# Kernel optimization log

Measured on AMD Instinct MI355X. Metric: run time of the kernel, lower is better.

## Reference

```python
import jax, jax.numpy as jnp
import numpy as np

N = 50000      # graph nodes
E = 800000     # edges
R = 8          # relations
D = 128        # entity_dim == relation_dim == n_hidden
L = 2          # gnn layers
NE = 150000    # entity vocab
NEG_SLOPE = 0.01


def setup_inputs() -> dict:
    key = jax.random.key(0)
    ks = jax.random.split(key, 9)
    return {
        "node_ids": jax.random.randint(ks[0], (N,), 0, NE),
        "relation_ids": jax.random.randint(ks[1], (E,), 0, R),
        "src": jax.random.randint(ks[2], (E,), 0, N),
        "dst": jax.random.randint(ks[3], (E,), 0, N),
        "entity_table": jax.random.normal(ks[4], (NE, D), dtype=jnp.float32) * 0.1,
        "relation_table": jax.random.normal(ks[5], (R, D), dtype=jnp.float32) * 0.1,
        "relation_W": jax.random.normal(ks[6], (R, D, D), dtype=jnp.float32) * 0.1,
        "res_fc_W": jax.random.normal(ks[7], (L, D, D), dtype=jnp.float32) * 0.1,
        "res_fc2_W": jax.random.normal(ks[8], (L, D, D), dtype=jnp.float32) * 0.1,
    }


def _kgat_layer(h, efeat, rel, src, dst, relation_W, W1, W2):
    # project every node by every relation weight: (N, R, D)
    proj = jnp.einsum('nd,rde->nre', h, relation_W)
    t_r = proj[src, rel]            # (E, D)  W_r h_src
    h_r = proj[dst, rel]            # (E, D)  W_r h_dst
    # att = (W_r h_t)^T tanh(W_r h_dst + e_r)
    att = jnp.sum(t_r * jnp.tanh(h_r + efeat), axis=1)  # (E,)
    # edge softmax over incoming edges of each dst node
    m = jax.ops.segment_max(att, dst, num_segments=N)
    ex = jnp.exp(att - m[dst])
    s = jax.ops.segment_sum(ex, dst, num_segments=N)
    a = ex / s[dst]                 # (E,)
    # message = a * h_src, scatter-sum to dst
    h_nb = jax.ops.segment_sum(h[src] * a[:, None], dst, num_segments=N)  # (N, D)
    out = (jax.nn.leaky_relu((h + h_nb) @ W1.T, NEG_SLOPE)
           + jax.nn.leaky_relu((h * h_nb) @ W2.T, NEG_SLOPE))
    return h_nb, out


def reference(node_ids, relation_ids, src, dst, entity_table, relation_table,
              relation_W, res_fc_W, res_fc2_W):
    h = entity_table[node_ids]           # (N, D)
    efeat = relation_table[relation_ids]  # (E, D)
    cache = [h]
    for i in range(L):
        h, out = _kgat_layer(h, efeat, relation_ids, src, dst,
                             relation_W, res_fc_W[i], res_fc2_W[i])
        cache.append(out)
    return jnp.concatenate(cache, axis=1)  # (N, D*(L+1))
```

## Files before the change

kernel.cpp:

```cpp
#include <hip/hip_runtime.h>
#include <math.h>

#define DDIM 128
#define RREL 8

typedef _Float16 f16;
typedef __attribute__((ext_vector_type(2))) _Float16 h2;
typedef __attribute__((ext_vector_type(8))) _Float16 f16x8;
typedef __attribute__((ext_vector_type(4))) float f32x4;

static __device__ __forceinline__ unsigned short f2h(float f) {
    union { _Float16 h; unsigned short s; } c; c.h = (_Float16)f; return c.s;
}
static __device__ __forceinline__ h2 u2h(unsigned u) {
    union { unsigned u; h2 h; } c; c.u = u; return c.h;
}
static __device__ __forceinline__ unsigned h2u(h2 h) {
    union { unsigned u; h2 h; } c; c.h = h; return c.u;
}
static __device__ __forceinline__ float lrelu(float x) {
    return x > 0.0f ? x : 0.01f * x;
}
static __device__ __forceinline__ float tanh_fast(float x) {
    float e = __expf(2.0f * x);
    return 1.0f - 2.0f * __builtin_amdgcn_rcpf(e + 1.0f);
}

__global__ __launch_bounds__(256) void prep_weights(const float* __restrict__ relW,
                                                    const float* __restrict__ fcW,
                                                    const float* __restrict__ fc2W,
                                                    unsigned short* __restrict__ Wt,
                                                    unsigned short* __restrict__ Wq,
                                                    unsigned short* __restrict__ Wb1,
                                                    unsigned short* __restrict__ Wb2) {
    int i = blockIdx.x * 256 + threadIdx.x;
    const int NT = RREL * DDIM * DDIM;
    const int NF = 2 * DDIM * DDIM;
    if (i < NT) {
        float w = relW[i];
        int r = i >> 14;
        int d = (i >> 7) & 127;
        int e = i & 127;
        unsigned short h = f2h(w);
        Wt[(r << 14) + (e << 7) + d] = h;
        Wq[i] = h;
    } else if (i < NT + NF) {
        int j = i - NT;
        Wb1[j] = f2h(fcW[j]);
    } else if (i < NT + 2 * NF) {
        int j = i - NT - NF;
        Wb2[j] = f2h(fc2W[j]);
    }
}

__global__ __launch_bounds__(256) void gather_h0(const int* __restrict__ node_ids,
                                                 const float* __restrict__ etab,
                                                 unsigned short* __restrict__ hb0,
                                                 float* __restrict__ out, int N) {
    int i = blockIdx.x * 256 + threadIdx.x;
    if (i >= N * 32) return;
    int n = i >> 5;
    int c4 = (i & 31) * 4;
    float4 v = *(const float4*)(etab + (size_t)node_ids[n] * DDIM + c4);
    *(float4*)(out + (size_t)n * 384 + c4) = v;
    unsigned lo = (unsigned)f2h(v.x) | ((unsigned)f2h(v.y) << 16);
    unsigned hi = (unsigned)f2h(v.z) | ((unsigned)f2h(v.w) << 16);
    *(uint2*)(hb0 + (size_t)n * DDIM + c4) = make_uint2(lo, hi);
}

__global__ __launch_bounds__(256) void hist_k(const int* __restrict__ dst,
                                              int* __restrict__ counts, int E) {
    int i = blockIdx.x * 256 + threadIdx.x;
    if (i < E) atomicAdd(counts + dst[i], 1);
}

__global__ __launch_bounds__(256) void scan_a(const int* __restrict__ counts,
                                              int* __restrict__ tmp,
                                              int* __restrict__ part, int N) {
    __shared__ int sh[256];
    int i = blockIdx.x * 256 + threadIdx.x;
    int v = (i < N) ? counts[i] : 0;
    sh[threadIdx.x] = v;
    __syncthreads();
    #pragma unroll
    for (int o = 1; o < 256; o <<= 1) {
        int t = (threadIdx.x >= o) ? sh[threadIdx.x - o] : 0;
        __syncthreads();
        sh[threadIdx.x] += t;
        __syncthreads();
    }
    if (i < N) tmp[i] = sh[threadIdx.x];
    if (threadIdx.x == 255) part[blockIdx.x] = sh[255];
}

__global__ __launch_bounds__(256) void scan_b(int* __restrict__ part, int nb) {
    __shared__ int sh[256];
    int v = (threadIdx.x < nb) ? part[threadIdx.x] : 0;
    sh[threadIdx.x] = v;
    __syncthreads();
    #pragma unroll
    for (int o = 1; o < 256; o <<= 1) {
        int t = (threadIdx.x >= o) ? sh[threadIdx.x - o] : 0;
        __syncthreads();
        sh[threadIdx.x] += t;
        __syncthreads();
    }
    if (threadIdx.x < nb) part[threadIdx.x] = sh[threadIdx.x] - v;
}

__global__ __launch_bounds__(256) void scan_c(const int* __restrict__ counts,
                                              const int* __restrict__ tmp,
                                              const int* __restrict__ part,
                                              int* __restrict__ row_ptr,
                                              int* __restrict__ woff, int N) {
    int i = blockIdx.x * 256 + threadIdx.x;
    if (i >= N) return;
    int incl = tmp[i] + part[blockIdx.x];
    row_ptr[i + 1] = incl;
    woff[i] = incl - counts[i];
    if (i == 0) row_ptr[0] = 0;
}

__global__ __launch_bounds__(256) void scatter_k(const int* __restrict__ src,
                                                 const int* __restrict__ rel,
                                                 const int* __restrict__ dst,
                                                 int* __restrict__ woff,
                                                 int2* __restrict__ epack, int E) {
    int i = blockIdx.x * 256 + threadIdx.x;
    if (i >= E) return;
    int p = atomicAdd(woff + dst[i], 1);
    epack[p] = make_int2(src[i], rel[i]);
}

__global__ __launch_bounds__(256) void prq_gemm(const unsigned short* __restrict__ hb,
                                                const unsigned short* __restrict__ Wt,
                                                const unsigned short* __restrict__ Wq,
                                                const float* __restrict__ rtab,
                                                unsigned short* __restrict__ qout, int N) {
    __shared__ __align__(16) unsigned short Ts[128][136];
    int tid = threadIdx.x;
    int row0 = blockIdx.x * 128;
    int r = blockIdx.y;

    int wave = tid >> 6, lane = tid & 63;
    int wr = wave >> 1, wc = wave & 1;
    int m = lane & 15, quad = lane >> 4;

    const unsigned short* WtR = Wt + (r << 14);
    const unsigned short* WqR = Wq + (r << 14);
    const unsigned short* hbase = hb + (size_t)(row0 + wr * 64 + m) * DDIM;

    f32x4 acc[4][4];
    #pragma unroll
    for (int mt = 0; mt < 4; ++mt)
        #pragma unroll
        for (int nt = 0; nt < 4; ++nt) acc[mt][nt] = (f32x4){0.f, 0.f, 0.f, 0.f};

    #pragma unroll
    for (int kk = 0; kk < 4; ++kk) {
        f16x8 af[4], bfr[4];
        #pragma unroll
        for (int i = 0; i < 4; ++i)
            bfr[i] = *(const f16x8*)(WtR + ((wc * 64 + i * 16 + m) << 7) + kk * 32 + quad * 8);
        #pragma unroll
        for (int i = 0; i < 4; ++i)
            af[i] = *(const f16x8*)(hbase + (size_t)(i * 16) * DDIM + kk * 32 + quad * 8);
        #pragma unroll
        for (int mt = 0; mt < 4; ++mt)
            #pragma unroll
            for (int nt = 0; nt < 4; ++nt)
                acc[mt][nt] = __builtin_amdgcn_mfma_f32_16x16x32_f16(af[mt], bfr[nt], acc[mt][nt], 0, 0, 0);
    }

    f16x8 bq[4][4];
    #pragma unroll
    for (int kk = 0; kk < 4; ++kk)
        #pragma unroll
        for (int i = 0; i < 4; ++i)
            bq[kk][i] = *(const f16x8*)(WqR + ((wc * 64 + i * 16 + m) << 7) + kk * 32 + quad * 8);

    float rv[4];
    #pragma unroll
    for (int nt = 0; nt < 4; ++nt)
        rv[nt] = rtab[r * DDIM + wc * 64 + nt * 16 + m];
    #pragma unroll
    for (int mt = 0; mt < 4; ++mt) {
        #pragma unroll
        for (int nt = 0; nt < 4; ++nt) {
            #pragma unroll
            for (int q = 0; q < 4; ++q) {
                int row = wr * 64 + mt * 16 + quad * 4 + q;
                int col = wc * 64 + nt * 16 + m;
                Ts[row][col] = f2h(tanh_fast(acc[mt][nt][q] + rv[nt]));
            }
        }
    }
    __syncthreads();

    #pragma unroll
    for (int mt = 0; mt < 4; ++mt)
        #pragma unroll
        for (int nt = 0; nt < 4; ++nt) acc[mt][nt] = (f32x4){0.f, 0.f, 0.f, 0.f};

    #pragma unroll
    for (int kk = 0; kk < 4; ++kk) {
        f16x8 af[4];
        #pragma unroll
        for (int i = 0; i < 4; ++i)
            af[i] = *(const f16x8*)(&Ts[wr * 64 + i * 16 + m][kk * 32 + quad * 8]);
        #pragma unroll
        for (int mt = 0; mt < 4; ++mt)
            #pragma unroll
            for (int nt = 0; nt < 4; ++nt)
                acc[mt][nt] = __builtin_amdgcn_mfma_f32_16x16x32_f16(af[mt], bq[kk][nt], acc[mt][nt], 0, 0, 0);
    }
    __syncthreads();

    #pragma unroll
    for (int mt = 0; mt < 4; ++mt) {
        #pragma unroll
        for (int nt = 0; nt < 4; ++nt) {
            #pragma unroll
            for (int q = 0; q < 4; ++q) {
                int row = wr * 64 + mt * 16 + quad * 4 + q;
                int col = wc * 64 + nt * 16 + m;
                Ts[row][col] = f2h(acc[mt][nt][q]);
            }
        }
    }
    __syncthreads();

    #pragma unroll
    for (int j = 0; j < 8; ++j) {
        int idx = j * 256 + tid;
        int row = idx >> 4;
        int c8 = (idx & 15) * 8;
        int grow = row0 + row;
        if (grow < N)
            *(uint4*)(qout + (size_t)grow * 1024 + (r << 7) + c8) = *(const uint4*)(&Ts[row][c8]);
    }
}

__global__ __launch_bounds__(256) void fused_agg(const unsigned short* __restrict__ qt,
                                                 const unsigned short* __restrict__ hb,
                                                 const int* __restrict__ row_ptr,
                                                 const int2* __restrict__ epack,
                                                 unsigned short* __restrict__ hbn, int N) {
    __shared__ __align__(16) unsigned q2[4][RREL][68];
    int wv = threadIdx.x >> 6, lane = threadIdx.x & 63;
    int n = blockIdx.x * 4 + wv;
    if (n >= N) return;
    int g  = lane >> 3;
    int gp = lane & 7;
    int dbase = gp * 16;

    #pragma unroll
    for (int r = 0; r < RREL; ++r)
        q2[wv][r][lane] = *(const unsigned*)(qt + (size_t)n * 1024 + r * 128 + lane * 2);

    int beg = row_ptr[n], end = row_ptr[n + 1];
    float s = 0.f;
    h2 a[8];
    #pragma unroll
    for (int i = 0; i < 8; ++i) a[i] = u2h(0u);

    for (int base = beg; base < end; base += 8) {
        int eidx = base + g;
        bool act = eidx < end;
        int2 ep = act ? epack[eidx] : make_int2(0, 0);
        int sr = ep.x, rr = ep.y;
        const unsigned short* hp = hb + (size_t)sr * DDIM + dbase;
        uint4 hv0 = *(const uint4*)(hp);
        uint4 hv1 = *(const uint4*)(hp + 8);
        const unsigned* tp = &q2[wv][rr][gp * 8];
        uint4 t0 = *(const uint4*)(tp);
        uint4 t1 = *(const uint4*)(tp + 4);

        h2 vs = u2h(hv0.x) * u2h(t0.x);
        vs += u2h(hv0.y) * u2h(t0.y);
        vs += u2h(hv0.z) * u2h(t0.z);
        vs += u2h(hv0.w) * u2h(t0.w);
        vs += u2h(hv1.x) * u2h(t1.x);
        vs += u2h(hv1.y) * u2h(t1.y);
        vs += u2h(hv1.z) * u2h(t1.z);
        vs += u2h(hv1.w) * u2h(t1.w);
        float v = (float)vs.x + (float)vs.y;
        v += __shfl_xor(v, 1, 64);
        v += __shfl_xor(v, 2, 64);
        v += __shfl_xor(v, 4, 64);

        float p = act ? __expf(fminf(v, 10.f)) : 0.f;
        s += p;
        h2 ph;
        ph.x = (_Float16)p;
        ph.y = ph.x;
        a[0] += ph * u2h(hv0.x);
        a[1] += ph * u2h(hv0.y);
        a[2] += ph * u2h(hv0.z);
        a[3] += ph * u2h(hv0.w);
        a[4] += ph * u2h(hv1.x);
        a[5] += ph * u2h(hv1.y);
        a[6] += ph * u2h(hv1.z);
        a[7] += ph * u2h(hv1.w);
    }

    #pragma unroll
    for (int st = 8; st < 64; st <<= 1) {
        s += __shfl_xor(s, st, 64);
        #pragma unroll
        for (int i = 0; i < 8; ++i) {
            unsigned t = (unsigned)__shfl_xor((int)h2u(a[i]), st, 64);
            a[i] += u2h(t);
        }
    }

    float inv = (end > beg) ? 1.0f / s : 0.0f;

    if (g == 0) {
        unsigned pk[8];
        #pragma unroll
        for (int i = 0; i < 8; ++i) {
            float lo = (float)a[i].x * inv;
            float hi = (float)a[i].y * inv;
            h2 o;
            o.x = (_Float16)lo;
            o.y = (_Float16)hi;
            pk[i] = h2u(o);
        }
        unsigned short* bp = hbn + (size_t)n * DDIM + gp * 16;
        *(uint4*)(bp)     = make_uint4(pk[0], pk[1], pk[2], pk[3]);
        *(uint4*)(bp + 8) = make_uint4(pk[4], pk[5], pk[6], pk[7]);
    }
}

__global__ __launch_bounds__(256) void out_gemm(const unsigned short* __restrict__ hb,
                                                const unsigned short* __restrict__ hbn,
                                                const unsigned short* __restrict__ W1,
                                                const unsigned short* __restrict__ W2,
                                                float* __restrict__ out,
                                                int colbase, int N) {
    __shared__ __align__(16) unsigned short As[64][136];
    __shared__ __align__(16) unsigned short Bs[128][136];
    int tid = threadIdx.x;
    int row0 = blockIdx.x * 64;
    int wave = tid >> 6, lane = tid & 63;
    int m = lane & 15, quad = lane >> 4;

    f32x4 acc[2][8];
    #pragma unroll
    for (int p = 0; p < 2; ++p)
        #pragma unroll
        for (int t = 0; t < 8; ++t) acc[p][t] = (f32x4){0.f, 0.f, 0.f, 0.f};

    #pragma unroll
    for (int p = 0; p < 2; ++p) {
        #pragma unroll
        for (int j = 0; j < 4; ++j) {
            int idx = j * 256 + tid;
            int row = idx >> 4;
            int c8 = (idx & 15) * 8;
            int grow = row0 + row;
            unsigned pk[4] = {0, 0, 0, 0};
            if (grow < N) {
                uint4 hv = *(const uint4*)(hb + (size_t)grow * DDIM + c8);
                uint4 nv = *(const uint4*)(hbn + (size_t)grow * DDIM + c8);
                unsigned hw[4] = {hv.x, hv.y, hv.z, hv.w};
                unsigned nw[4] = {nv.x, nv.y, nv.z, nv.w};
                #pragma unroll
                for (int jj = 0; jj < 4; ++jj) {
                    h2 hh = u2h(hw[jj]), nn = u2h(nw[jj]);
                    h2 r = p ? (h2)(hh * nn) : (h2)(hh + nn);
                    pk[jj] = h2u(r);
                }
            }
            *(uint4*)(&As[row][c8]) = make_uint4(pk[0], pk[1], pk[2], pk[3]);
        }
        const unsigned short* W = p ? W2 : W1;
        #pragma unroll
        for (int j = 0; j < 8; ++j) {
            int idx = j * 256 + tid;
            int brow = idx >> 4;
            int c8 = (idx & 15) * 8;
            *(uint4*)(&Bs[brow][c8]) = *(const uint4*)(W + ((size_t)brow << 7) + c8);
        }
        __syncthreads();

        #pragma unroll
        for (int kk = 0; kk < 4; ++kk) {
            f16x8 av = *(const f16x8*)(&As[wave * 16 + m][kk * 32 + quad * 8]);
            #pragma unroll
            for (int t = 0; t < 8; ++t) {
                f16x8 b = *(const f16x8*)(&Bs[t * 16 + m][kk * 32 + quad * 8]);
                acc[p][t] = __builtin_amdgcn_mfma_f32_16x16x32_f16(av, b, acc[p][t], 0, 0, 0);
            }
        }
        __syncthreads();
    }

    #pragma unroll
    for (int t = 0; t < 8; ++t) {
        #pragma unroll
        for (int q = 0; q < 4; ++q) {
            int row = row0 + wave * 16 + quad * 4 + q;
            int col = t * 16 + m;
            if (row < N)
                out[(size_t)row * 384 + colbase + col] =
                    lrelu(acc[0][t][q]) + lrelu(acc[1][t][q]);
        }
    }
}

extern "C" void kernel_launch(void* const* d_in, const int* in_sizes, int n_in,
                              void* d_out, int out_size, void* d_ws, size_t ws_size,
                              hipStream_t stream) {
    const int* node_ids = (const int*)d_in[0];
    const int* rel_ids  = (const int*)d_in[1];
    const int* src      = (const int*)d_in[2];
    const int* dst      = (const int*)d_in[3];
    const float* etab   = (const float*)d_in[4];
    const float* rtab   = (const float*)d_in[5];
    const float* relW   = (const float*)d_in[6];
    const float* fcW    = (const float*)d_in[7];
    const float* fc2W   = (const float*)d_in[8];
    float* out = (float*)d_out;

    const int N = in_sizes[0];
    const int E = in_sizes[1];
    const int NB = (N + 255) / 256;

    char* ws = (char*)d_ws;
    size_t off = 0;
    auto alloc = [&](size_t bytes) -> char* {
        char* p = ws + off;
        off = (off + bytes + 255) & ~(size_t)255;
        return p;
    };
    unsigned short* hb[3];
    hb[0] = (unsigned short*)alloc((size_t)N * DDIM * 2);
    hb[1] = (unsigned short*)alloc((size_t)N * DDIM * 2);
    hb[2] = (unsigned short*)alloc((size_t)N * DDIM * 2);
    unsigned short* Wt  = (unsigned short*)alloc((size_t)RREL * DDIM * DDIM * 2);
    unsigned short* Wq  = (unsigned short*)alloc((size_t)RREL * DDIM * DDIM * 2);
    unsigned short* Wb1 = (unsigned short*)alloc((size_t)2 * DDIM * DDIM * 2);
    unsigned short* Wb2 = (unsigned short*)alloc((size_t)2 * DDIM * DDIM * 2);
    unsigned short* qt  = (unsigned short*)alloc((size_t)N * RREL * DDIM * 2);
    int*  counts  = (int*)alloc((size_t)N * 4);
    int*  tmp     = (int*)alloc((size_t)N * 4);
    int*  part    = (int*)alloc((size_t)NB * 4);
    int*  row_ptr = (int*)alloc((size_t)(N + 1) * 4);
    int*  woff    = (int*)alloc((size_t)N * 4);
    int2* epack   = (int2*)alloc((size_t)E * 8);

    const int NW = RREL * DDIM * DDIM + 4 * DDIM * DDIM;
    hipLaunchKernelGGL(prep_weights, dim3((NW + 255) / 256), dim3(256), 0, stream,
                       relW, fcW, fc2W, Wt, Wq, Wb1, Wb2);
    hipLaunchKernelGGL(gather_h0, dim3((N * 32 + 255) / 256), dim3(256), 0, stream,
                       node_ids, etab, hb[0], out, N);

    hipMemsetAsync(counts, 0, (size_t)N * 4, stream);
    hipLaunchKernelGGL(hist_k, dim3((E + 255) / 256), dim3(256), 0, stream, dst, counts, E);
    hipLaunchKernelGGL(scan_a, dim3(NB), dim3(256), 0, stream, counts, tmp, part, N);
    hipLaunchKernelGGL(scan_b, dim3(1), dim3(256), 0, stream, part, NB);
    hipLaunchKernelGGL(scan_c, dim3(NB), dim3(256), 0, stream, counts, tmp, part, row_ptr, woff, N);
    hipLaunchKernelGGL(scatter_k, dim3((E + 255) / 256), dim3(256), 0, stream,
                       src, rel_ids, dst, woff, epack, E);

    for (int l = 0; l < 2; ++l) {
        hipLaunchKernelGGL(prq_gemm, dim3((N + 127) / 128, 8), dim3(256), 0, stream,
                           hb[l], Wt, Wq, rtab, qt, N);
        hipLaunchKernelGGL(fused_agg, dim3((N + 3) / 4), dim3(256), 0, stream,
                           qt, hb[l], row_ptr, epack, hb[l + 1], N);
        hipLaunchKernelGGL(out_gemm, dim3((N + 63) / 64), dim3(256), 0, stream,
                           hb[l], hb[l + 1], Wb1 + (size_t)l * DDIM * DDIM, Wb2 + (size_t)l * DDIM * DDIM,
                           out, (l + 1) * DDIM, N);
    }
}
```

Before: 524.1 us.

## Stage h tile in LDS and loop over relations inside prq_gemm block

The projection kernel now loads a 64-row h tile once into shared memory and iterates over all 8 relations inside one block, instead of launching one block per (128-row tile, relation) pair that re-reads h from global memory. The output is written directly from accumulators as scattered 2-byte stores rather than staged through LDS for 16-byte coalesced stores. This cuts repeated global reads of h but shrinks parallelism, so each block runs 8 sequential relation passes, and the narrow uncoalesced stores to the large q output may hurt write bandwidth.

```diff
diff --git a/kernel.cpp b/kernel.cpp
--- a/kernel.cpp
+++ b/kernel.cpp
@@ -137,107 +137,114 @@
                                                 const unsigned short* __restrict__ Wq,
                                                 const float* __restrict__ rtab,
                                                 unsigned short* __restrict__ qout, int N) {
-    __shared__ __align__(16) unsigned short Ts[128][136];
+    __shared__ __align__(16) unsigned short Ah[64][136];
+    __shared__ __align__(16) unsigned short Ts[64][136];
     int tid = threadIdx.x;
-    int row0 = blockIdx.x * 128;
-    int r = blockIdx.y;
-
-    int wave = tid >> 6, lane = tid & 63;
-    int wr = wave >> 1, wc = wave & 1;
-    int m = lane & 15, quad = lane >> 4;
-
-    const unsigned short* WtR = Wt + (r << 14);
-    const unsigned short* WqR = Wq + (r << 14);
-    const unsigned short* hbase = hb + (size_t)(row0 + wr * 64 + m) * DDIM;
-
-    f32x4 acc[4][4];
-    #pragma unroll
-    for (int mt = 0; mt < 4; ++mt)
-        #pragma unroll
-        for (int nt = 0; nt < 4; ++nt) acc[mt][nt] = (f32x4){0.f, 0.f, 0.f, 0.f};
-
-    #pragma unroll
-    for (int kk = 0; kk < 4; ++kk) {
-        f16x8 af[4], bfr[4];
-        #pragma unroll
-        for (int i = 0; i < 4; ++i)
-            bfr[i] = *(const f16x8*)(WtR + ((wc * 64 + i * 16 + m) << 7) + kk * 32 + quad * 8);
-        #pragma unroll
-        for (int i = 0; i < 4; ++i)
-            af[i] = *(const f16x8*)(hbase + (size_t)(i * 16) * DDIM + kk * 32 + quad * 8);
-        #pragma unroll
-        for (int mt = 0; mt < 4; ++mt)
-            #pragma unroll
-            for (int nt = 0; nt < 4; ++nt)
-                acc[mt][nt] = __builtin_amdgcn_mfma_f32_16x16x32_f16(af[mt], bfr[nt], acc[mt][nt], 0, 0, 0);
-    }
-
-    f16x8 bq[4][4];
-    #pragma unroll
-    for (int kk = 0; kk < 4; ++kk)
-        #pragma unroll
-        for (int i = 0; i < 4; ++i)
-            bq[kk][i] = *(const f16x8*)(WqR + ((wc * 64 + i * 16 + m) << 7) + kk * 32 + quad * 8);
-
-    float rv[4];
-    #pragma unroll
-    for (int nt = 0; nt < 4; ++nt)
-        rv[nt] = rtab[r * DDIM + wc * 64 + nt * 16 + m];
-    #pragma unroll
-    for (int mt = 0; mt < 4; ++mt) {
-        #pragma unroll
-        for (int nt = 0; nt < 4; ++nt) {
-            #pragma unroll
-            for (int q = 0; q < 4; ++q) {
-                int row = wr * 64 + mt * 16 + quad * 4 + q;
-                int col = wc * 64 + nt * 16 + m;
-                Ts[row][col] = f2h(tanh_fast(acc[mt][nt][q] + rv[nt]));
-            }
-        }
-    }
-    __syncthreads();
-
-    #pragma unroll
-    for (int mt = 0; mt < 4; ++mt)
-        #pragma unroll
-        for (int nt = 0; nt < 4; ++nt) acc[mt][nt] = (f32x4){0.f, 0.f, 0.f, 0.f};
-
-    #pragma unroll
-    for (int kk = 0; kk < 4; ++kk) {
-        f16x8 af[4];
-        #pragma unroll
-        for (int i = 0; i < 4; ++i)
-            af[i] = *(const f16x8*)(&Ts[wr * 64 + i * 16 + m][kk * 32 + quad * 8]);
-        #pragma unroll
-        for (int mt = 0; mt < 4; ++mt)
-            #pragma unroll
-            for (int nt = 0; nt < 4; ++nt)
-                acc[mt][nt] = __builtin_amdgcn_mfma_f32_16x16x32_f16(af[mt], bq[kk][nt], acc[mt][nt], 0, 0, 0);
-    }
-    __syncthreads();
-
-    #pragma unroll
-    for (int mt = 0; mt < 4; ++mt) {
-        #pragma unroll
-        for (int nt = 0; nt < 4; ++nt) {
-            #pragma unroll
-            for (int q = 0; q < 4; ++q) {
-                int row = wr * 64 + mt * 16 + quad * 4 + q;
-                int col = wc * 64 + nt * 16 + m;
-                Ts[row][col] = f2h(acc[mt][nt][q]);
-            }
-        }
-    }
-    __syncthreads();
-
-    #pragma unroll
-    for (int j = 0; j < 8; ++j) {
+    int row0 = blockIdx.x * 64;
+
+    #pragma unroll
+    for (int j = 0; j < 4; ++j) {
         int idx = j * 256 + tid;
         int row = idx >> 4;
         int c8 = (idx & 15) * 8;
         int grow = row0 + row;
-        if (grow < N)
-            *(uint4*)(qout + (size_t)grow * 1024 + (r << 7) + c8) = *(const uint4*)(&Ts[row][c8]);
+        uint4 v = make_uint4(0, 0, 0, 0);
+        if (grow < N) v = *(const uint4*)(hb + (size_t)grow * DDIM + c8);
+        *(uint4*)(&Ah[row][c8]) = v;
+    }
+    __syncthreads();
+
+    int wave = tid >> 6, lane = tid & 63;
+    int wr = wave >> 1, wc = wave & 1;
+    int m = lane & 15, quad = lane >> 4;
+    const int rbase = wr * 32;
+    const int cbase = wc * 64;
+
+    for (int r = 0; r < RREL; ++r) {
+        const unsigned short* WtR = Wt + (r << 14);
+        const unsigned short* WqR = Wq + (r << 14);
+
+        f32x4 acc[2][4];
+        #pragma unroll
+        for (int mt = 0; mt < 2; ++mt)
+            #pragma unroll
+            for (int nt = 0; nt < 4; ++nt) acc[mt][nt] = (f32x4){0.f, 0.f, 0.f, 0.f};
+
+        #pragma unroll
+        for (int kk = 0; kk < 4; ++kk) {
+            f16x8 af[2], bfr[4];
+            #pragma unroll
+            for (int i = 0; i < 4; ++i)
+                bfr[i] = *(const f16x8*)(WtR + ((cbase + i * 16 + m) << 7) + kk * 32 + quad * 8);
+            #pragma unroll
+            for (int i = 0; i < 2; ++i)
+                af[i] = *(const f16x8*)(&Ah[rbase + i * 16 + m][kk * 32 + quad * 8]);
+            #pragma unroll
+            for (int mt = 0; mt < 2; ++mt)
+                #pragma unroll
+                for (int nt = 0; nt < 4; ++nt)
+                    acc[mt][nt] = __builtin_amdgcn_mfma_f32_16x16x32_f16(af[mt], bfr[nt], acc[mt][nt], 0, 0, 0);
+        }
+
+        f16x8 bq[4][4];
+        #pragma unroll
+        for (int kk = 0; kk < 4; ++kk)
+            #pragma unroll
+            for (int i = 0; i < 4; ++i)
+                bq[kk][i] = *(const f16x8*)(WqR + ((cbase + i * 16 + m) << 7) + kk * 32 + quad * 8);
+
+        float rv[4];
+        #pragma unroll
+        for (int nt = 0; nt < 4; ++nt)
+            rv[nt] = rtab[r * DDIM + cbase + nt * 16 + m];
+
+        __syncthreads();
+
+        #pragma unroll
+        for (int mt = 0; mt < 2; ++mt) {
+            #pragma unroll
+            for (int nt = 0; nt < 4; ++nt) {
+                #pragma unroll
+                for (int q = 0; q < 4; ++q) {
+                    int row = rbase + mt * 16 + quad * 4 + q;
+                    int col = cbase + nt * 16 + m;
+                    Ts[row][col] = f2h(tanh_fast(acc[mt][nt][q] + rv[nt]));
+                }
+            }
+        }
+        __syncthreads();
+
+        #pragma unroll
+        for (int mt = 0; mt < 2; ++mt)
+            #pragma unroll
+            for (int nt = 0; nt < 4; ++nt) acc[mt][nt] = (f32x4){0.f, 0.f, 0.f, 0.f};
+
+        #pragma unroll
+        for (int kk = 0; kk < 4; ++kk) {
+            f16x8 af[2];
+            #pragma unroll
+            for (int i = 0; i < 2; ++i)
+                af[i] = *(const f16x8*)(&Ts[rbase + i * 16 + m][kk * 32 + quad * 8]);
+            #pragma unroll
+            for (int mt = 0; mt < 2; ++mt)
+                #pragma unroll
+                for (int nt = 0; nt < 4; ++nt)
+                    acc[mt][nt] = __builtin_amdgcn_mfma_f32_16x16x32_f16(af[mt], bq[kk][nt], acc[mt][nt], 0, 0, 0);
+        }
+
+        #pragma unroll
+        for (int mt = 0; mt < 2; ++mt) {
+            #pragma unroll
+            for (int nt = 0; nt < 4; ++nt) {
+                #pragma unroll
+                for (int q = 0; q < 4; ++q) {
+                    int grow = row0 + rbase + mt * 16 + quad * 4 + q;
+                    int col = cbase + nt * 16 + m;
+                    if (grow < N)
+                        qout[(size_t)grow * 1024 + (r << 7) + col] = f2h(acc[mt][nt][q]);
+                }
+            }
+        }
     }
 }
 
@@ -466,7 +473,7 @@
                        src, rel_ids, dst, woff, epack, E);
 
     for (int l = 0; l < 2; ++l) {
-        hipLaunchKernelGGL(prq_gemm, dim3((N + 127) / 128, 8), dim3(256), 0, stream,
+        hipLaunchKernelGGL(prq_gemm, dim3((N + 63) / 64), dim3(256), 0, stream,
                            hb[l], Wt, Wq, rtab, qt, N);
         hipLaunchKernelGGL(fused_agg, dim3((N + 3) / 4), dim3(256), 0, stream,
                            qt, hb[l], row_ptr, epack, hb[l + 1], N);
```

Result: slower. 639.5 us (+22.0%).

## Give each wave full-width 32-row tile in prq_gemm to drop block barriers

Applied to the files above, without the earlier changes.

Rewrites the per-relation two-stage GEMM so each wave owns 32 full rows (all 128 columns) instead of a 64x64 quadrant. The intermediate tanh tile and output staging then stay private to each wave in shared memory, so the block-wide __syncthreads calls are removed, and out-of-range rows are zero-filled. The trade-off is that each wave must now load the full weight matrices, which doubles per-wave B-fragment traffic. Loading Wq per kk instead of preloading it lowers register pressure.

```diff
diff --git a/kernel.cpp b/kernel.cpp
--- a/kernel.cpp
+++ b/kernel.cpp
@@ -137,107 +137,91 @@
                                                 const unsigned short* __restrict__ Wq,
                                                 const float* __restrict__ rtab,
                                                 unsigned short* __restrict__ qout, int N) {
-    __shared__ __align__(16) unsigned short Ts[128][136];
+    __shared__ __align__(16) unsigned short Ts[4][32][136];
     int tid = threadIdx.x;
-    int row0 = blockIdx.x * 128;
+    int wave = tid >> 6, lane = tid & 63;
+    int m = lane & 15, quad = lane >> 4;
     int r = blockIdx.y;
-
-    int wave = tid >> 6, lane = tid & 63;
-    int wr = wave >> 1, wc = wave & 1;
-    int m = lane & 15, quad = lane >> 4;
+    int row0 = blockIdx.x * 128 + wave * 32;
 
     const unsigned short* WtR = Wt + (r << 14);
     const unsigned short* WqR = Wq + (r << 14);
-    const unsigned short* hbase = hb + (size_t)(row0 + wr * 64 + m) * DDIM;
-
-    f32x4 acc[4][4];
-    #pragma unroll
-    for (int mt = 0; mt < 4; ++mt)
-        #pragma unroll
-        for (int nt = 0; nt < 4; ++nt) acc[mt][nt] = (f32x4){0.f, 0.f, 0.f, 0.f};
+
+    const f16x8 zf = (f16x8){0, 0, 0, 0, 0, 0, 0, 0};
+
+    f32x4 acc[2][8];
+    #pragma unroll
+    for (int i = 0; i < 2; ++i)
+        #pragma unroll
+        for (int j = 0; j < 8; ++j) acc[i][j] = (f32x4){0.f, 0.f, 0.f, 0.f};
 
     #pragma unroll
     for (int kk = 0; kk < 4; ++kk) {
-        f16x8 af[4], bfr[4];
-        #pragma unroll
-        for (int i = 0; i < 4; ++i)
-            bfr[i] = *(const f16x8*)(WtR + ((wc * 64 + i * 16 + m) << 7) + kk * 32 + quad * 8);
-        #pragma unroll
-        for (int i = 0; i < 4; ++i)
-            af[i] = *(const f16x8*)(hbase + (size_t)(i * 16) * DDIM + kk * 32 + quad * 8);
-        #pragma unroll
-        for (int mt = 0; mt < 4; ++mt)
+        f16x8 bfr[8], af[2];
+        #pragma unroll
+        for (int j = 0; j < 8; ++j)
+            bfr[j] = *(const f16x8*)(WtR + ((j * 16 + m) << 7) + kk * 32 + quad * 8);
+        #pragma unroll
+        for (int i = 0; i < 2; ++i) {
+            int grow = row0 + i * 16 + m;
+            af[i] = (grow < N) ? *(const f16x8*)(hb + (size_t)grow * DDIM + kk * 32 + quad * 8) : zf;
+        }
+        #pragma unroll
+        for (int i = 0; i < 2; ++i)
             #pragma unroll
-            for (int nt = 0; nt < 4; ++nt)
-                acc[mt][nt] = __builtin_amdgcn_mfma_f32_16x16x32_f16(af[mt], bfr[nt], acc[mt][nt], 0, 0, 0);
-    }
-
-    f16x8 bq[4][4];
-    #pragma unroll
-    for (int kk = 0; kk < 4; ++kk)
-        #pragma unroll
-        for (int i = 0; i < 4; ++i)
-            bq[kk][i] = *(const f16x8*)(WqR + ((wc * 64 + i * 16 + m) << 7) + kk * 32 + quad * 8);
-
-    float rv[4];
-    #pragma unroll
-    for (int nt = 0; nt < 4; ++nt)
-        rv[nt] = rtab[r * DDIM + wc * 64 + nt * 16 + m];
-    #pragma unroll
-    for (int mt = 0; mt < 4; ++mt) {
-        #pragma unroll
-        for (int nt = 0; nt < 4; ++nt) {
+            for (int j = 0; j < 8; ++j)
+                acc[i][j] = __builtin_amdgcn_mfma_f32_16x16x32_f16(af[i], bfr[j], acc[i][j], 0, 0, 0);
+    }
+
+    float rv[8];
+    #pragma unroll
+    for (int j = 0; j < 8; ++j)
+        rv[j] = rtab[r * DDIM + j * 16 + m];
+    #pragma unroll
+    for (int i = 0; i < 2; ++i)
+        #pragma unroll
+        for (int j = 0; j < 8; ++j)
             #pragma unroll
-            for (int q = 0; q < 4; ++q) {
-                int row = wr * 64 + mt * 16 + quad * 4 + q;
-                int col = wc * 64 + nt * 16 + m;
-                Ts[row][col] = f2h(tanh_fast(acc[mt][nt][q] + rv[nt]));
-            }
-        }
-    }
-    __syncthreads();
-
-    #pragma unroll
-    for (int mt = 0; mt < 4; ++mt)
-        #pragma unroll
-        for (int nt = 0; nt < 4; ++nt) acc[mt][nt] = (f32x4){0.f, 0.f, 0.f, 0.f};
+            for (int q = 0; q < 4; ++q)
+                Ts[wave][i * 16 + quad * 4 + q][j * 16 + m] = f2h(tanh_fast(acc[i][j][q] + rv[j]));
+
+    #pragma unroll
+    for (int i = 0; i < 2; ++i)
+        #pragma unroll
+        for (int j = 0; j < 8; ++j) acc[i][j] = (f32x4){0.f, 0.f, 0.f, 0.f};
 
     #pragma unroll
     for (int kk = 0; kk < 4; ++kk) {
-        f16x8 af[4];
-        #pragma unroll
-        for (int i = 0; i < 4; ++i)
-            af[i] = *(const f16x8*)(&Ts[wr * 64 + i * 16 + m][kk * 32 + quad * 8]);
-        #pragma unroll
-        for (int mt = 0; mt < 4; ++mt)
+        f16x8 bq[8], af[2];
+        #pragma unroll
+        for (int j = 0; j < 8; ++j)
+            bq[j] = *(const f16x8*)(WqR + ((j * 16 + m) << 7) + kk * 32 + quad * 8);
+        #pragma unroll
+        for (int i = 0; i < 2; ++i)
+            af[i] = *(const f16x8*)(&Ts[wave][i * 16 + m][kk * 32 + quad * 8]);
+        #pragma unroll
+        for (int i = 0; i < 2; ++i)
             #pragma unroll
-            for (int nt = 0; nt < 4; ++nt)
-                acc[mt][nt] = __builtin_amdgcn_mfma_f32_16x16x32_f16(af[mt], bq[kk][nt], acc[mt][nt], 0, 0, 0);
-    }
-    __syncthreads();
-
-    #pragma unroll
-    for (int mt = 0; mt < 4; ++mt) {
-        #pragma unroll
-        for (int nt = 0; nt < 4; ++nt) {
+            for (int j = 0; j < 8; ++j)
+                acc[i][j] = __builtin_amdgcn_mfma_f32_16x16x32_f16(af[i], bq[j], acc[i][j], 0, 0, 0);
+    }
+
+    #pragma unroll
+    for (int i = 0; i < 2; ++i)
+        #pragma unroll
+        for (int j = 0; j < 8; ++j)
             #pragma unroll
-            for (int q = 0; q < 4; ++q) {
-                int row = wr * 64 + mt * 16 + quad * 4 + q;
-                int col = wc * 64 + nt * 16 + m;
-                Ts[row][col] = f2h(acc[mt][nt][q]);
-            }
-        }
-    }
-    __syncthreads();
-
-    #pragma unroll
-    for (int j = 0; j < 8; ++j) {
-        int idx = j * 256 + tid;
+            for (int q = 0; q < 4; ++q)
+                Ts[wave][i * 16 + quad * 4 + q][j * 16 + m] = f2h(acc[i][j][q]);
+
+    #pragma unroll
+    for (int it = 0; it < 8; ++it) {
+        int idx = it * 64 + lane;
         int row = idx >> 4;
         int c8 = (idx & 15) * 8;
         int grow = row0 + row;
         if (grow < N)
-            *(uint4*)(qout + (size_t)grow * 1024 + (r << 7) + c8) = *(const uint4*)(&Ts[row][c8]);
+            *(uint4*)(qout + (size_t)grow * 1024 + (r << 7) + c8) = *(const uint4*)(&Ts[wave][row][c8]);
     }
 }
 
```

New measurement: 583.3 us. 11.3% more time.
